# Kernel tuning notes

Measured on AMD Instinct MI355X. Metric: run time of the kernel, lower is better.

## Reference

```python
import jax, jax.numpy as jnp
import numpy as np

N_HEAD = 16
RMS_EPS = 1.1920928955078125e-07  # torch F.rms_norm default eps = finfo(fp32).eps


def _rope_tables(seq_len, head_dim, dtype):
    steps = jnp.arange(seq_len, dtype=jnp.float32)
    rates = 10000.0 ** (-jnp.arange(0, head_dim, 2, dtype=jnp.float32) / head_dim)
    angles = jnp.outer(steps, rates)  # [S, D/2]
    return jnp.cos(angles).astype(dtype)[None, None], jnp.sin(angles).astype(dtype)[None, None]


def _apply_rotary(x, cos, sin):
    # interleaved RoPE: pairs (x[2i], x[2i+1]) rotated
    left = x[..., ::2]
    right = x[..., 1::2]
    lo = left * cos - right * sin
    ro = left * sin + right * cos
    return jnp.stack((lo, ro), axis=-1).reshape(x.shape)


def _rms_norm(x, eps=RMS_EPS):
    ms = jnp.mean(jnp.square(x), axis=-1, keepdims=True)
    return x * jax.lax.rsqrt(ms + eps)


def setup_inputs() -> dict:
    key = jax.random.key(0)
    k1, k2, k3 = jax.random.split(key, 3)
    B, S, E = 2, 2048, 2048
    x = jax.random.normal(k1, (B, S, E), dtype=jnp.float32)
    w_qkv = jax.random.normal(k2, (3 * E, E), dtype=jnp.float32) * (E ** -0.5)
    w_proj = jax.random.normal(k3, (E, E), dtype=jnp.float32) * (E ** -0.5)
    return {"x": x, "w_qkv": w_qkv, "w_proj": w_proj}


def reference(x, w_qkv, w_proj):
    B, S, E = x.shape
    H = N_HEAD
    D = E // H

    qkv = x @ w_qkv.T  # [B, S, 3E]
    q, k, v = jnp.split(qkv, 3, axis=-1)
    # [B, S, E] -> [B, H, S, D]
    q = q.reshape(B, S, H, D).transpose(0, 2, 1, 3)
    k = k.reshape(B, S, H, D).transpose(0, 2, 1, 3)
    v = v.reshape(B, S, H, D).transpose(0, 2, 1, 3)

    cos, sin = _rope_tables(S, D, x.dtype)  # [1,1,S,D/2]
    q = _apply_rotary(q, cos, sin)
    k = _apply_rotary(k, cos, sin)

    q = _rms_norm(q)
    k = _rms_norm(k)

    scale = 1.0 / jnp.sqrt(jnp.asarray(D, dtype=x.dtype))
    scores = jnp.einsum("bhqd,bhkd->bhqk", q, k) * scale  # [B,H,S,S]
    causal = jnp.tril(jnp.ones((S, S), dtype=bool))
    scores = jnp.where(causal[None, None], scores, jnp.asarray(-jnp.inf, dtype=scores.dtype))
    attn = jax.nn.softmax(scores, axis=-1)
    y = jnp.einsum("bhqk,bhkd->bhqd", attn, v)  # [B,H,S,D]
    y = y.transpose(0, 2, 1, 3).reshape(B, S, E)
    return y @ w_proj.T
```

## Files before the change

kernel.cpp:

```cpp
#include <hip/hip_runtime.h>

typedef unsigned short ushort_t;
using bf16x8 = __attribute__((ext_vector_type(8))) short;
using u16x8  = __attribute__((ext_vector_type(8))) unsigned short;
using f32x4  = __attribute__((ext_vector_type(4))) float;

#define DEV static __device__ __forceinline__

DEV unsigned short f2bf(float f) {
  union { float f; unsigned u; } a; a.f = f;
  unsigned r = a.u + 0x7fffu + ((a.u >> 16) & 1u);
  return (unsigned short)(r >> 16);
}
DEV float bf2f(unsigned short u) {
  union { unsigned u; float f; } a; a.u = ((unsigned)u) << 16;
  return a.f;
}
DEV void load_lds16(const void* g, void* l) {
  __builtin_amdgcn_global_load_lds(
      (const __attribute__((address_space(1))) void*)g,
      (__attribute__((address_space(3))) void*)l, 16, 0, 0);
}

__global__ __launch_bounds__(256) void cast_kernel(
    const float* __restrict__ src, ushort_t* __restrict__ dst, int n4) {
  int i = blockIdx.x * 256 + threadIdx.x;
  if (i >= n4) return;
  float4 f = ((const float4*)src)[i];
  ushort4 o;
  o.x = f2bf(f.x); o.y = f2bf(f.y); o.z = f2bf(f.z); o.w = f2bf(f.w);
  ((ushort4*)dst)[i] = o;
}

__global__ __launch_bounds__(256) void rope_tables_kernel(float* __restrict__ tab) {
  int idx = blockIdx.x * 256 + threadIdx.x;
  int s = idx >> 6, i = idx & 63;
  float rate = exp2f(-13.287712379549449f * ((float)(2 * i) * (1.0f / 128.0f)));
  float ang = (float)s * rate;
  tab[idx * 2]     = cosf(ang);
  tab[idx * 2 + 1] = sinf(ang);
}

template<int BN, int OUTF32>
__global__ __launch_bounds__(512) void gemm8p(
    const ushort_t* __restrict__ A, const ushort_t* __restrict__ B,
    void* __restrict__ C, int M, int N, int K) {
  constexpr int NF      = BN / 64;
  constexpr int NSPAN   = BN / 4;
  constexpr int SLOT_A  = 256 * 32;
  constexpr int SLOT_B  = BN * 32;
  constexpr int SLOT    = SLOT_A + SLOT_B;
  constexpr int LOADS_B = BN / 128;
  constexpr int VMC     = (2 + LOADS_B) * 3;
  __shared__ __align__(16) ushort_t lds[4 * SLOT];

  const int nby = M >> 8;
  const int nbx = N / BN;
  const int nwg = nby * nbx;
  const int orig = blockIdx.x;
  const int wgid = (orig & 7) * (nwg >> 3) + (orig >> 3);
  const int by = wgid % nby;
  const int bx = wgid / nby;
  const int bm = by * 256, bn = bx * BN;

  const int tid = threadIdx.x;
  const int wave = tid >> 6, lane = tid & 63;
  const int ql = lane & 15, lk = lane >> 4;
  const int wm = wave >> 2, wn = wave & 3;

  f32x4 acc[8][NF];
#pragma unroll
  for (int m = 0; m < 8; ++m)
#pragma unroll
    for (int n = 0; n < NF; ++n) acc[m][n] = (f32x4){0.f, 0.f, 0.f, 0.f};

  const int srow = tid >> 2;
  const int scol = (tid & 3) * 16;
  const int sswz = scol ^ (((srow >> 1) & 3) << 4);
  const size_t rbA = (size_t)(K * 2);
  const char* aS0 = (const char*)A + (size_t)(bm + srow) * rbA + sswz;
  const char* aS1 = (const char*)A + (size_t)(bm + srow + 128) * rbA + sswz;
  const char* bS0 = (const char*)B + (size_t)(bn + srow) * rbA + sswz;
  const char* bS1 = (const char*)B + (size_t)(bn + srow + 128) * rbA + sswz;
  char* ldsc = (char*)lds;
  const int dA0 = tid * 16;
  const int dA1 = tid * 16 + 8192;
  const int dB0 = SLOT_A * 2 + tid * 16;
  const int dB1 = SLOT_A * 2 + tid * 16 + 8192;

#define ISSUE(KS, SL) do {                                   \
    const size_t ko = (size_t)(KS) * 64;                     \
    char* sb = ldsc + (SL) * (SLOT * 2);                     \
    load_lds16(aS0 + ko, sb + dA0);                          \
    load_lds16(aS1 + ko, sb + dA1);                          \
    load_lds16(bS0 + ko, sb + dB0);                          \
    if (LOADS_B == 2) load_lds16(bS1 + ko, sb + dB1);        \
  } while (0)

  const int qswz = ((ql >> 1) & 3) << 4;
  const int fcol = (lk * 16) ^ qswz;
  const int aOff = (wm * 128 + ql) * 64 + fcol;
  const int bOff = SLOT_A * 2 + (wn * NSPAN + ql) * 64 + fcol;

  const int ns = K >> 5;
  ISSUE(0, 0); ISSUE(1, 1); ISSUE(2, 2);

  for (int s = 0; s < ns; ++s) {
    int kn = s + 3; if (kn >= ns) kn = ns - 1;
    ISSUE(kn, (s + 3) & 3);
    if (VMC == 12) asm volatile("s_waitcnt vmcnt(12)" ::: "memory");
    else           asm volatile("s_waitcnt vmcnt(9)"  ::: "memory");
    asm volatile("s_barrier" ::: "memory");

    const char* sb = ldsc + (s & 3) * (SLOT * 2);
    bf16x8 af[8], bfr[NF];
#pragma unroll
    for (int m = 0; m < 8; ++m) af[m] = *(const bf16x8*)(sb + aOff + m * 1024);
#pragma unroll
    for (int n = 0; n < NF; ++n) bfr[n] = *(const bf16x8*)(sb + bOff + n * 1024);

    __builtin_amdgcn_s_setprio(1);
#pragma unroll
    for (int m = 0; m < 8; ++m)
#pragma unroll
      for (int n = 0; n < NF; ++n)
        acc[m][n] = __builtin_amdgcn_mfma_f32_16x16x32_bf16(af[m], bfr[n], acc[m][n], 0, 0, 0);
    __builtin_amdgcn_s_setprio(0);
    asm volatile("s_barrier" ::: "memory");
  }
  asm volatile("s_waitcnt vmcnt(0)" ::: "memory");
#undef ISSUE

#pragma unroll
  for (int m = 0; m < 8; ++m)
#pragma unroll
    for (int i = 0; i < 4; ++i) {
      const size_t row = (size_t)(bm + wm * 128 + m * 16 + lk * 4 + i);
#pragma unroll
      for (int n = 0; n < NF; ++n) {
        const size_t col = (size_t)(bn + wn * NSPAN + n * 16 + ql);
        float v = acc[m][n][i];
        if (OUTF32) ((float*)C)[row * (size_t)N + col] = v;
        else        ((ushort_t*)C)[row * (size_t)N + col] = f2bf(v);
      }
    }
}

__global__ __launch_bounds__(256) void rope_rms_kernel(
    const ushort_t* __restrict__ qkv, ushort_t* __restrict__ q,
    ushort_t* __restrict__ k, ushort_t* __restrict__ vt,
    const float* __restrict__ tab) {
  const int lane = threadIdx.x & 63;
  const int row  = blockIdx.x * 4 + (threadIdx.x >> 6);
  const int h = row & 15;
  int t = row >> 4;
  const int which = t % 3; t /= 3;
  const int s = t & 2047;
  const int b = t >> 11;
  const size_t src = ((size_t)(b * 2048 + s)) * 6144 + which * 2048 + h * 128 + lane * 2;
  ushort2 xv = *(const ushort2*)&qkv[src];
  if (which == 2) {
    size_t vbase = ((size_t)((b * 16 + h) * 128 + lane * 2)) * 2048 + s;
    vt[vbase]        = xv.x;
    vt[vbase + 2048] = xv.y;
    return;
  }
  float lo = bf2f(xv.x), ro = bf2f(xv.y);
  const float2 cs = *(const float2*)&tab[(s * 64 + lane) * 2];
  float l2 = lo * cs.x - ro * cs.y;
  float r2 = lo * cs.y + ro * cs.x;
  float ss = l2 * l2 + r2 * r2;
#pragma unroll
  for (int off = 1; off < 64; off <<= 1) ss += __shfl_xor(ss, off);
  float inv = rsqrtf(ss * (1.0f / 128.0f) + 1.1920928955078125e-07f);
  if (which == 0) inv *= 0.1275174398f;
  lo = l2 * inv; ro = r2 * inv;
  ushort_t* dst = (which == 0) ? q : k;
  ushort2 o; o.x = f2bf(lo); o.y = f2bf(ro);
  *(ushort2*)&dst[(((size_t)(b * 16 + h)) * 2048 + s) * 128 + lane * 2] = o;
}

__global__ __launch_bounds__(256) void attn_kernel(
    const ushort_t* __restrict__ Q, const ushort_t* __restrict__ K,
    const ushort_t* __restrict__ VT, ushort_t* __restrict__ Y) {
  __shared__ __align__(16) ushort_t sK[64 * 128];
  __shared__ __align__(16) ushort_t sV[128 * 64];
  const int bh = blockIdx.x;
  const int yp = blockIdx.y;
  const int wave = threadIdx.x >> 6, lane = threadIdx.x & 63;
  const int ql = lane & 15, lk = lane >> 4;
  const size_t hq = (size_t)bh * 2048 * 128;
  const int b = bh >> 4, h = bh & 15;

  const char* kB = (const char*)(K + hq);
  const char* vB = (const char*)(VT + hq);
  const char* kSrc[4]; char* kDst[4];
  const char* vSrc[4]; char* vDst[4];
#pragma unroll
  for (int t = 0; t < 4; ++t) {
    int r = wave * 16 + t * 4 + (lane >> 4);
    int kgr = r >> 4, lkr = (r >> 2) & 3, ir = r & 3;
    int rho = (kgr >> 1) * 32 + lkr * 8 + (kgr & 1) * 4 + ir;
    kSrc[t] = kB + rho * 256 + (((lane & 15) * 16) ^ ((r & 7) << 4));
    kDst[t] = (char*)sK + (wave * 256 + t * 64 + lane) * 16;
    int d = wave * 32 + t * 8 + (lane >> 3);
    vSrc[t] = vB + (size_t)d * 4096 + (((lane & 7) * 16) ^ ((d & 7) << 4));
    vDst[t] = (char*)sV + (wave * 256 + t * 64 + lane) * 16;
  }

  for (int pass = 0; pass < 2; ++pass) {
    const int qt = pass ? (31 - yp) : yp;
    const int q = qt * 64 + wave * 16 + ql;

    bf16x8 qf[4];
#pragma unroll
    for (int ks = 0; ks < 4; ++ks)
      qf[ks] = *(const bf16x8*)&Q[hq + (size_t)q * 128 + ks * 32 + lk * 8];

    f32x4 acc[8];
#pragma unroll
    for (int g = 0; g < 8; ++g) acc[g] = (f32x4){0.f, 0.f, 0.f, 0.f};
    float mrow = -3.0e38f, lsum = 0.f;

    for (int kt = 0; kt <= qt; ++kt) {
#pragma unroll
      for (int t = 0; t < 4; ++t) {
        load_lds16(kSrc[t] + (size_t)kt * 16384, kDst[t]);
        load_lds16(vSrc[t] + kt * 128, vDst[t]);
      }
      __syncthreads();

      f32x4 st[4];
#pragma unroll
      for (int kg = 0; kg < 4; ++kg) st[kg] = (f32x4){0.f, 0.f, 0.f, 0.f};
#pragma unroll
      for (int kg = 0; kg < 4; ++kg) {
        const int row = kg * 16 + ql;
        const int rswz = (row & 7) << 4;
#pragma unroll
        for (int ks = 0; ks < 4; ++ks) {
          bf16x8 kf = *(const bf16x8*)((const char*)sK + row * 256 + ((ks * 64 + lk * 16) ^ rswz));
          st[kg] = __builtin_amdgcn_mfma_f32_16x16x32_bf16(kf, qf[ks], st[kg], 0, 0, 0);
        }
      }
      float sv[4][4]; float mp = -3.0e38f;
#pragma unroll
      for (int kg = 0; kg < 4; ++kg) {
        const int kl = ((kg >> 1) << 5) + lk * 8 + ((kg & 1) << 2);
#pragma unroll
        for (int i = 0; i < 4; ++i) {
          const int key = kt * 64 + kl + i;
          float v = (key <= q) ? st[kg][i] : -3.0e38f;
          sv[kg][i] = v;
          mp = fmaxf(mp, v);
        }
      }
      mp = fmaxf(mp, __shfl_xor(mp, 16));
      mp = fmaxf(mp, __shfl_xor(mp, 32));
      const float mn = fmaxf(mrow, mp);
      const float corr = exp2f(mrow - mn);
      mrow = mn;
      float p[4][4]; float rs = 0.f;
#pragma unroll
      for (int kg = 0; kg < 4; ++kg)
#pragma unroll
        for (int i = 0; i < 4; ++i) {
          float e = exp2f(sv[kg][i] - mn);
          p[kg][i] = e; rs += e;
        }
      rs += __shfl_xor(rs, 16);
      rs += __shfl_xor(rs, 32);
      lsum = lsum * corr + rs;
#pragma unroll
      for (int g = 0; g < 8; ++g)
#pragma unroll
        for (int i = 0; i < 4; ++i) acc[g][i] *= corr;
      bf16x8 pb[2];
#pragma unroll
      for (int c = 0; c < 2; ++c) {
        union { bf16x8 v; ushort_t u[8]; } pk;
#pragma unroll
        for (int j = 0; j < 8; ++j) pk.u[j] = f2bf(p[2 * c + (j >> 2)][j & 3]);
        pb[c] = pk.v;
      }
#pragma unroll
      for (int dg = 0; dg < 8; ++dg) {
        const int d = dg * 16 + ql;
        const int dswz = (d & 7) << 4;
#pragma unroll
        for (int c = 0; c < 2; ++c) {
          bf16x8 vf = *(const bf16x8*)((const char*)sV + d * 128 + ((c * 64 + lk * 16) ^ dswz));
          acc[dg] = __builtin_amdgcn_mfma_f32_16x16x32_bf16(vf, pb[c], acc[dg], 0, 0, 0);
        }
      }
      __syncthreads();
    }

    const float inv = 1.0f / lsum;
    const size_t orow = ((size_t)(b * 2048 + q)) * 2048 + h * 128;
#pragma unroll
    for (int dg = 0; dg < 8; ++dg) {
      ushort4 o;
      o.x = f2bf(acc[dg][0] * inv);
      o.y = f2bf(acc[dg][1] * inv);
      o.z = f2bf(acc[dg][2] * inv);
      o.w = f2bf(acc[dg][3] * inv);
      *(ushort4*)&Y[orow + dg * 16 + lk * 4] = o;
    }
  }
}

extern "C" void kernel_launch(void* const* d_in, const int* in_sizes, int n_in,
                              void* d_out, int out_size, void* d_ws, size_t ws_size,
                              hipStream_t stream) {
  const float* x     = (const float*)d_in[0];
  const float* wqkv  = (const float*)d_in[1];
  const float* wproj = (const float*)d_in[2];
  float* out = (float*)d_out;
  char* ws = (char*)d_ws;

  ushort_t* x_bf     = (ushort_t*)(ws);
  ushort_t* wqkv_bf  = (ushort_t*)(ws + 16777216);
  ushort_t* wproj_bf = (ushort_t*)(ws + 41943040);
  ushort_t* qkv_bf   = (ushort_t*)(ws + 50331648);
  ushort_t* q_bf     = (ushort_t*)(ws + 100663296);
  ushort_t* k_bf     = (ushort_t*)(ws + 117440512);
  ushort_t* vt_bf    = (ushort_t*)(ws + 134217728);
  float*    tab      = (float*)(ws + 150994944);
  if (ws_size < 152043520u) return;

  cast_kernel<<<8192, 256, 0, stream>>>(x, x_bf, 2097152);
  cast_kernel<<<12288, 256, 0, stream>>>(wqkv, wqkv_bf, 3145728);
  cast_kernel<<<4096, 256, 0, stream>>>(wproj, wproj_bf, 1048576);
  rope_tables_kernel<<<512, 256, 0, stream>>>(tab);

  gemm8p<256, 0><<<384, 512, 0, stream>>>(x_bf, wqkv_bf, qkv_bf, 4096, 6144, 2048);

  rope_rms_kernel<<<49152, 256, 0, stream>>>(qkv_bf, q_bf, k_bf, vt_bf, tab);

  attn_kernel<<<dim3(32, 16), 256, 0, stream>>>(q_bf, k_bf, vt_bf, qkv_bf );

  gemm8p<128, 1><<<256, 512, 0, stream>>>(qkv_bf, wproj_bf, out, 4096, 2048, 2048);
}
```

Baseline: 317.8 us.

## Double-buffer A fragments in registers and retile GEMM waves

The GEMM main loop now prefetches the next k-step's A fragments from LDS into a second register set while the MFMAs for the current step run, unrolling by two to ping-pong the buffers. The waitcnt is relaxed to allow two outstanding stages. For BN=128 the wave layout changes to 4x2 with 64-row warp tiles, and launch bounds request two blocks per CU. The aim is to hide LDS read latency behind MFMAs, at the cost of more registers, and to better balance the projection GEMM.

```diff
diff --git a/kernel.cpp b/kernel.cpp
--- a/kernel.cpp
+++ b/kernel.cpp
@@ -42,103 +42,119 @@
 }
 
 template<int BN, int OUTF32>
-__global__ __launch_bounds__(512) void gemm8p(
+__global__ __launch_bounds__(512, 2) void gemm_dp(
     const ushort_t* __restrict__ A, const ushort_t* __restrict__ B,
     void* __restrict__ C, int M, int N, int K) {
-  constexpr int NF      = BN / 64;
-  constexpr int NSPAN   = BN / 4;
+  constexpr int WROWS   = (BN == 256) ? 128 : 64;
+  constexpr int MF      = WROWS / 16;
+  constexpr int NF      = 4;
   constexpr int SLOT_A  = 256 * 32;
   constexpr int SLOT_B  = BN * 32;
-  constexpr int SLOT    = SLOT_A + SLOT_B;
+  constexpr int SLOTB   = (SLOT_A + SLOT_B) * 2;
   constexpr int LOADS_B = BN / 128;
-  constexpr int VMC     = (2 + LOADS_B) * 3;
-  __shared__ __align__(16) ushort_t lds[4 * SLOT];
+  __shared__ __align__(16) ushort_t lds[4 * (SLOT_A + SLOT_B)];
 
   const int nby = M >> 8;
-  const int nbx = N / BN;
-  const int nwg = nby * nbx;
+  const int nwg = nby * (N / BN);
   const int orig = blockIdx.x;
   const int wgid = (orig & 7) * (nwg >> 3) + (orig >> 3);
-  const int by = wgid % nby;
-  const int bx = wgid / nby;
-  const int bm = by * 256, bn = bx * BN;
+  const int bm = (wgid % nby) * 256;
+  const int bn = (wgid / nby) * BN;
 
   const int tid = threadIdx.x;
   const int wave = tid >> 6, lane = tid & 63;
   const int ql = lane & 15, lk = lane >> 4;
-  const int wm = wave >> 2, wn = wave & 3;
-
-  f32x4 acc[8][NF];
-#pragma unroll
-  for (int m = 0; m < 8; ++m)
+  const int wm = (BN == 256) ? (wave >> 2) : (wave >> 1);
+  const int wn = (BN == 256) ? (wave & 3) : (wave & 1);
+
+  f32x4 acc[MF][NF];
+#pragma unroll
+  for (int m = 0; m < MF; ++m)
 #pragma unroll
     for (int n = 0; n < NF; ++n) acc[m][n] = (f32x4){0.f, 0.f, 0.f, 0.f};
 
   const int srow = tid >> 2;
-  const int scol = (tid & 3) * 16;
-  const int sswz = scol ^ (((srow >> 1) & 3) << 4);
+  const int sswz = ((tid & 3) * 16) ^ (((srow >> 1) & 3) << 4);
   const size_t rbA = (size_t)(K * 2);
   const char* aS0 = (const char*)A + (size_t)(bm + srow) * rbA + sswz;
   const char* aS1 = (const char*)A + (size_t)(bm + srow + 128) * rbA + sswz;
   const char* bS0 = (const char*)B + (size_t)(bn + srow) * rbA + sswz;
-  const char* bS1 = (const char*)B + (size_t)(bn + srow + 128) * rbA + sswz;
+  const char* bS1 = (LOADS_B == 2)
+      ? (const char*)B + (size_t)(bn + srow + 128) * rbA + sswz : bS0;
   char* ldsc = (char*)lds;
   const int dA0 = tid * 16;
   const int dA1 = tid * 16 + 8192;
   const int dB0 = SLOT_A * 2 + tid * 16;
   const int dB1 = SLOT_A * 2 + tid * 16 + 8192;
 
-#define ISSUE(KS, SL) do {                                   \
-    const size_t ko = (size_t)(KS) * 64;                     \
-    char* sb = ldsc + (SL) * (SLOT * 2);                     \
-    load_lds16(aS0 + ko, sb + dA0);                          \
-    load_lds16(aS1 + ko, sb + dA1);                          \
-    load_lds16(bS0 + ko, sb + dB0);                          \
-    if (LOADS_B == 2) load_lds16(bS1 + ko, sb + dB1);        \
+  const int fcol = (lk * 16) ^ (((ql >> 1) & 3) << 4);
+  const int aOff = (wm * WROWS + ql) * 64 + fcol;
+  const int bOff = SLOT_A * 2 + (wn * 64 + ql) * 64 + fcol;
+
+  const int ns = K >> 5;
+
+#define STEP(S, CUR, NXT) do {                                                  \
+    int kn_ = (S) + 3; if (kn_ > ns - 1) kn_ = ns - 1;                          \
+    const size_t ko_ = (size_t)kn_ * 64;                                        \
+    char* sb_ = ldsc + (((S) + 3) & 3) * SLOTB;                                 \
+    load_lds16(aS0 + ko_, sb_ + dA0);                                           \
+    load_lds16(aS1 + ko_, sb_ + dA1);                                           \
+    load_lds16(bS0 + ko_, sb_ + dB0);                                           \
+    if (LOADS_B == 2) load_lds16(bS1 + ko_, sb_ + dB1);                         \
+    asm volatile("s_waitcnt vmcnt(%0)" :: "n"(2 * (2 + LOADS_B)) : "memory");   \
+    __builtin_amdgcn_s_barrier();                                               \
+    asm volatile("" ::: "memory");                                              \
+    const char* sbc_ = ldsc + ((S) & 3) * SLOTB;                                \
+    const char* sbn_ = ldsc + (((S) + 1) & 3) * SLOTB;                          \
+    bf16x8 bfr_[NF];                                                            \
+    _Pragma("unroll")                                                           \
+    for (int n = 0; n < NF; ++n)                                                \
+      bfr_[n] = *(const bf16x8*)(sbc_ + bOff + n * 1024);                       \
+    _Pragma("unroll")                                                           \
+    for (int m = 0; m < MF; ++m)                                                \
+      NXT[m] = *(const bf16x8*)(sbn_ + aOff + m * 1024);                        \
+    __builtin_amdgcn_s_setprio(1);                                              \
+    _Pragma("unroll")                                                           \
+    for (int n = 0; n < NF; ++n)                                                \
+      _Pragma("unroll")                                                         \
+      for (int m = 0; m < MF; ++m)                                              \
+        acc[m][n] = __builtin_amdgcn_mfma_f32_16x16x32_bf16(CUR[m], bfr_[n],    \
+                                                            acc[m][n], 0, 0, 0);\
+    __builtin_amdgcn_s_setprio(0);                                              \
+    __builtin_amdgcn_s_barrier();                                               \
   } while (0)
 
-  const int qswz = ((ql >> 1) & 3) << 4;
-  const int fcol = (lk * 16) ^ qswz;
-  const int aOff = (wm * 128 + ql) * 64 + fcol;
-  const int bOff = SLOT_A * 2 + (wn * NSPAN + ql) * 64 + fcol;
-
-  const int ns = K >> 5;
-  ISSUE(0, 0); ISSUE(1, 1); ISSUE(2, 2);
-
-  for (int s = 0; s < ns; ++s) {
-    int kn = s + 3; if (kn >= ns) kn = ns - 1;
-    ISSUE(kn, (s + 3) & 3);
-    if (VMC == 12) asm volatile("s_waitcnt vmcnt(12)" ::: "memory");
-    else           asm volatile("s_waitcnt vmcnt(9)"  ::: "memory");
-    asm volatile("s_barrier" ::: "memory");
-
-    const char* sb = ldsc + (s & 3) * (SLOT * 2);
-    bf16x8 af[8], bfr[NF];
-#pragma unroll
-    for (int m = 0; m < 8; ++m) af[m] = *(const bf16x8*)(sb + aOff + m * 1024);
-#pragma unroll
-    for (int n = 0; n < NF; ++n) bfr[n] = *(const bf16x8*)(sb + bOff + n * 1024);
-
-    __builtin_amdgcn_s_setprio(1);
-#pragma unroll
-    for (int m = 0; m < 8; ++m)
-#pragma unroll
-      for (int n = 0; n < NF; ++n)
-        acc[m][n] = __builtin_amdgcn_mfma_f32_16x16x32_bf16(af[m], bfr[n], acc[m][n], 0, 0, 0);
-    __builtin_amdgcn_s_setprio(0);
-    asm volatile("s_barrier" ::: "memory");
+#pragma unroll
+  for (int i = 0; i < 3; ++i) {
+    const size_t ko = (size_t)i * 64;
+    char* sb = ldsc + i * SLOTB;
+    load_lds16(aS0 + ko, sb + dA0);
+    load_lds16(aS1 + ko, sb + dA1);
+    load_lds16(bS0 + ko, sb + dB0);
+    if (LOADS_B == 2) load_lds16(bS1 + ko, sb + dB1);
+  }
+  asm volatile("s_waitcnt vmcnt(%0)" :: "n"(2 * (2 + LOADS_B)) : "memory");
+  __builtin_amdgcn_s_barrier();
+  asm volatile("" ::: "memory");
+  bf16x8 frA[MF], frB[MF];
+#pragma unroll
+  for (int m = 0; m < MF; ++m) frA[m] = *(const bf16x8*)(ldsc + aOff + m * 1024);
+
+  for (int s = 0; s < ns; s += 2) {
+    STEP(s, frA, frB);
+    STEP(s + 1, frB, frA);
   }
   asm volatile("s_waitcnt vmcnt(0)" ::: "memory");
-#undef ISSUE
-
-#pragma unroll
-  for (int m = 0; m < 8; ++m)
+#undef STEP
+
+#pragma unroll
+  for (int m = 0; m < MF; ++m)
 #pragma unroll
     for (int i = 0; i < 4; ++i) {
-      const size_t row = (size_t)(bm + wm * 128 + m * 16 + lk * 4 + i);
+      const size_t row = (size_t)(bm + wm * WROWS + m * 16 + lk * 4 + i);
 #pragma unroll
       for (int n = 0; n < NF; ++n) {
-        const size_t col = (size_t)(bn + wn * NSPAN + n * 16 + ql);
+        const size_t col = (size_t)(bn + wn * 64 + n * 16 + ql);
         float v = acc[m][n][i];
         if (OUTF32) ((float*)C)[row * (size_t)N + col] = v;
         else        ((ushort_t*)C)[row * (size_t)N + col] = f2bf(v);
@@ -334,11 +350,11 @@
   cast_kernel<<<4096, 256, 0, stream>>>(wproj, wproj_bf, 1048576);
   rope_tables_kernel<<<512, 256, 0, stream>>>(tab);
 
-  gemm8p<256, 0><<<384, 512, 0, stream>>>(x_bf, wqkv_bf, qkv_bf, 4096, 6144, 2048);
+  gemm_dp<256, 0><<<384, 512, 0, stream>>>(x_bf, wqkv_bf, qkv_bf, 4096, 6144, 2048);
 
   rope_rms_kernel<<<49152, 256, 0, stream>>>(qkv_bf, q_bf, k_bf, vt_bf, tab);
 
   attn_kernel<<<dim3(32, 16), 256, 0, stream>>>(q_bf, k_bf, vt_bf, qkv_bf );
 
-  gemm8p<128, 1><<<256, 512, 0, stream>>>(qkv_bf, wproj_bf, out, 4096, 2048, 2048);
-}
+  gemm_dp<128, 1><<<256, 512, 0, stream>>>(qkv_bf, wproj_bf, out, 4096, 2048, 2048);
+}
```

Measured after the change: 313.6 us. No clear change (-1.3%).

## Restructure GEMM into double-buffered 64-wide K tiles with interleaved load/MFMA phases

Applied to the files above, without the earlier changes.

Replaces the 4-stage ring buffer of 32-wide K slices with a 2-buffer pipeline over 64-wide K tiles. Each tile is split into four MFMA phases, with LDS fragment reads and the next tile's global-to-LDS loads interleaved between barriers. The LDS swizzle changes to an 8-way XOR over 128-byte rows, and launch bounds request 2 workgroups per CU. This aims to hide load latency and raise MFMA utilisation. In exchange it adds many more barriers, and occupancy 2 may be limited by LDS size and register count. An unused mfma16 prototype is declared but never defined.

```diff
diff --git a/kernel.cpp b/kernel.cpp
--- a/kernel.cpp
+++ b/kernel.cpp
@@ -21,6 +21,7 @@
       (const __attribute__((address_space(1))) void*)g,
       (__attribute__((address_space(3))) void*)l, 16, 0, 0);
 }
+DEV bf16x8 mfma16(bf16x8 a, bf16x8 b);
 
 __global__ __launch_bounds__(256) void cast_kernel(
     const float* __restrict__ src, ushort_t* __restrict__ dst, int n4) {
@@ -42,29 +43,25 @@
 }
 
 template<int BN, int OUTF32>
-__global__ __launch_bounds__(512) void gemm8p(
-    const ushort_t* __restrict__ A, const ushort_t* __restrict__ B,
+__global__ __launch_bounds__(512, 2) void gemm8(
+    const ushort_t* __restrict__ A, const ushort_t* __restrict__ Bm,
     void* __restrict__ C, int M, int N, int K) {
-  constexpr int NF      = BN / 64;
-  constexpr int NSPAN   = BN / 4;
-  constexpr int SLOT_A  = 256 * 32;
-  constexpr int SLOT_B  = BN * 32;
-  constexpr int SLOT    = SLOT_A + SLOT_B;
-  constexpr int LOADS_B = BN / 128;
-  constexpr int VMC     = (2 + LOADS_B) * 3;
-  __shared__ __align__(16) ushort_t lds[4 * SLOT];
+  constexpr int NF   = BN / 64;
+  constexpr int ABY  = 256 * 64 * 2;
+  constexpr int BBY  = BN * 64 * 2;
+  constexpr int BUFB = ABY + BBY;
+  __shared__ __align__(16) char lds[2 * BUFB];
 
   const int nby = M >> 8;
-  const int nbx = N / BN;
-  const int nwg = nby * nbx;
+  const int nwg = nby * (N / BN);
   const int orig = blockIdx.x;
   const int wgid = (orig & 7) * (nwg >> 3) + (orig >> 3);
-  const int by = wgid % nby;
-  const int bx = wgid / nby;
-  const int bm = by * 256, bn = bx * BN;
+  const int bm = (wgid % nby) * 256;
+  const int bn = (wgid / nby) * BN;
 
   const int tid = threadIdx.x;
-  const int wave = tid >> 6, lane = tid & 63;
+  const int lane = tid & 63;
+  const int wave = tid >> 6;
   const int ql = lane & 15, lk = lane >> 4;
   const int wm = wave >> 2, wn = wave & 3;
 
@@ -74,62 +71,172 @@
 #pragma unroll
     for (int n = 0; n < NF; ++n) acc[m][n] = (f32x4){0.f, 0.f, 0.f, 0.f};
 
-  const int srow = tid >> 2;
-  const int scol = (tid & 3) * 16;
-  const int sswz = scol ^ (((srow >> 1) & 3) << 4);
-  const size_t rbA = (size_t)(K * 2);
-  const char* aS0 = (const char*)A + (size_t)(bm + srow) * rbA + sswz;
-  const char* aS1 = (const char*)A + (size_t)(bm + srow + 128) * rbA + sswz;
-  const char* bS0 = (const char*)B + (size_t)(bn + srow) * rbA + sswz;
-  const char* bS1 = (const char*)B + (size_t)(bn + srow + 128) * rbA + sswz;
-  char* ldsc = (char*)lds;
-  const int dA0 = tid * 16;
-  const int dA1 = tid * 16 + 8192;
-  const int dB0 = SLOT_A * 2 + tid * 16;
-  const int dB1 = SLOT_A * 2 + tid * 16 + 8192;
-
-#define ISSUE(KS, SL) do {                                   \
-    const size_t ko = (size_t)(KS) * 64;                     \
-    char* sb = ldsc + (SL) * (SLOT * 2);                     \
-    load_lds16(aS0 + ko, sb + dA0);                          \
-    load_lds16(aS1 + ko, sb + dA1);                          \
-    load_lds16(bS0 + ko, sb + dB0);                          \
-    if (LOADS_B == 2) load_lds16(bS1 + ko, sb + dB1);        \
-  } while (0)
-
-  const int qswz = ((ql >> 1) & 3) << 4;
-  const int fcol = (lk * 16) ^ qswz;
-  const int aOff = (wm * 128 + ql) * 64 + fcol;
-  const int bOff = SLOT_A * 2 + (wn * NSPAN + ql) * 64 + fcol;
-
-  const int ns = K >> 5;
-  ISSUE(0, 0); ISSUE(1, 1); ISSUE(2, 2);
-
-  for (int s = 0; s < ns; ++s) {
-    int kn = s + 3; if (kn >= ns) kn = ns - 1;
-    ISSUE(kn, (s + 3) & 3);
-    if (VMC == 12) asm volatile("s_waitcnt vmcnt(12)" ::: "memory");
-    else           asm volatile("s_waitcnt vmcnt(9)"  ::: "memory");
-    asm volatile("s_barrier" ::: "memory");
-
-    const char* sb = ldsc + (s & 3) * (SLOT * 2);
-    bf16x8 af[8], bfr[NF];
-#pragma unroll
-    for (int m = 0; m < 8; ++m) af[m] = *(const bf16x8*)(sb + aOff + m * 1024);
-#pragma unroll
-    for (int n = 0; n < NF; ++n) bfr[n] = *(const bf16x8*)(sb + bOff + n * 1024);
-
-    __builtin_amdgcn_s_setprio(1);
-#pragma unroll
-    for (int m = 0; m < 8; ++m)
-#pragma unroll
-      for (int n = 0; n < NF; ++n)
-        acc[m][n] = __builtin_amdgcn_mfma_f32_16x16x32_bf16(af[m], bfr[n], acc[m][n], 0, 0, 0);
-    __builtin_amdgcn_s_setprio(0);
-    asm volatile("s_barrier" ::: "memory");
+  const int srow = tid >> 3;
+  const int scol = ((tid & 7) ^ (srow & 7)) * 16;
+  const size_t rb = (size_t)K * 2;
+  const char* aS[4];
+#pragma unroll
+  for (int c = 0; c < 4; ++c)
+    aS[c] = (const char*)A + (size_t)(bm + c * 64 + srow) * rb + scol;
+  const char* bS[NF];
+#pragma unroll
+  for (int c = 0; c < NF; ++c)
+    bS[c] = (const char*)Bm + (size_t)(bn + c * 64 + srow) * rb + scol;
+  char* const ldsc = (char*)lds;
+  const int dT = tid * 16;
+
+  const int aRow = wm * 128 + ql;
+  const int bRow = wn * (BN / 4) + ql;
+  const int qx = ql & 7;
+
+#define RDA(BUF, m, kh) \
+  (*(const bf16x8*)((BUF) + (aRow + (m) * 16) * 128 + ((((kh) << 2) | lk) ^ qx) * 16))
+#define RDB(BUF, n, kh) \
+  (*(const bf16x8*)((BUF) + ABY + (bRow + (n) * 16) * 128 + ((((kh) << 2) | lk) ^ qx) * 16))
+#define STGA(BUF, KT, c) load_lds16(aS[c] + (size_t)(KT) * 128, (BUF) + (c) * 8192 + dT)
+#define STGB(BUF, KT, c) load_lds16(bS[c] + (size_t)(KT) * 128, (BUF) + ABY + (c) * 8192 + dT)
+#define MFMA(a, b, c) __builtin_amdgcn_mfma_f32_16x16x32_bf16(a, b, c, 0, 0, 0)
+
+  const int ns = K >> 6;
+
+  STGA(ldsc, 0, 0); STGA(ldsc, 0, 2);
+  STGB(ldsc, 0, 0); STGB(ldsc, 0, 1);
+  if constexpr (NF == 4) { STGB(ldsc, 0, 2); STGB(ldsc, 0, 3); }
+  STGA(ldsc, 0, 1); STGA(ldsc, 0, 3);
+  asm volatile("s_waitcnt vmcnt(2)" ::: "memory");
+  __builtin_amdgcn_s_barrier();
+
+  for (int t = 0; t < ns; ++t) {
+    char* bufR = ldsc + (t & 1) * BUFB;
+    char* bufW = ldsc + ((t + 1) & 1) * BUFB;
+    const int kn = (t + 1 < ns) ? t + 1 : ns - 1;
+
+    if constexpr (NF == 4) {
+      bf16x8 aF[4][2], bF[4][2];
+#pragma unroll
+      for (int mi = 0; mi < 4; ++mi) {
+        aF[mi][0] = RDA(bufR, mi, 0); aF[mi][1] = RDA(bufR, mi, 1);
+      }
+#pragma unroll
+      for (int n = 0; n < 2; ++n) {
+        bF[n][0] = RDB(bufR, n, 0); bF[n][1] = RDB(bufR, n, 1);
+      }
+      STGA(bufW, kn, 0); STGA(bufW, kn, 2);
+      STGB(bufW, kn, 0); STGB(bufW, kn, 1); STGB(bufW, kn, 2); STGB(bufW, kn, 3);
+      __builtin_amdgcn_s_barrier();
+      __builtin_amdgcn_s_setprio(1);
+#pragma unroll
+      for (int n = 0; n < 2; ++n)
+#pragma unroll
+        for (int kh = 0; kh < 2; ++kh)
+#pragma unroll
+          for (int mi = 0; mi < 4; ++mi)
+            acc[mi][n] = MFMA(aF[mi][kh], bF[n][kh], acc[mi][n]);
+      __builtin_amdgcn_s_setprio(0);
+      __builtin_amdgcn_s_barrier();
+#pragma unroll
+      for (int n = 2; n < 4; ++n) {
+        bF[n][0] = RDB(bufR, n, 0); bF[n][1] = RDB(bufR, n, 1);
+      }
+      asm volatile("s_waitcnt vmcnt(6)" ::: "memory");
+      __builtin_amdgcn_s_barrier();
+      __builtin_amdgcn_s_setprio(1);
+#pragma unroll
+      for (int n = 2; n < 4; ++n)
+#pragma unroll
+        for (int kh = 0; kh < 2; ++kh)
+#pragma unroll
+          for (int mi = 0; mi < 4; ++mi)
+            acc[mi][n] = MFMA(aF[mi][kh], bF[n][kh], acc[mi][n]);
+      __builtin_amdgcn_s_setprio(0);
+      __builtin_amdgcn_s_barrier();
+#pragma unroll
+      for (int mi = 0; mi < 4; ++mi) {
+        aF[mi][0] = RDA(bufR, 4 + mi, 0); aF[mi][1] = RDA(bufR, 4 + mi, 1);
+      }
+      STGA(bufW, kn, 1); STGA(bufW, kn, 3);
+      __builtin_amdgcn_s_barrier();
+      __builtin_amdgcn_s_setprio(1);
+#pragma unroll
+      for (int n = 0; n < 2; ++n)
+#pragma unroll
+        for (int kh = 0; kh < 2; ++kh)
+#pragma unroll
+          for (int mi = 0; mi < 4; ++mi)
+            acc[4 + mi][n] = MFMA(aF[mi][kh], bF[n][kh], acc[4 + mi][n]);
+      __builtin_amdgcn_s_setprio(0);
+      __builtin_amdgcn_s_barrier();
+      __builtin_amdgcn_s_setprio(1);
+#pragma unroll
+      for (int n = 2; n < 4; ++n)
+#pragma unroll
+        for (int kh = 0; kh < 2; ++kh)
+#pragma unroll
+          for (int mi = 0; mi < 4; ++mi)
+            acc[4 + mi][n] = MFMA(aF[mi][kh], bF[n][kh], acc[4 + mi][n]);
+      __builtin_amdgcn_s_setprio(0);
+      asm volatile("s_waitcnt vmcnt(2)" ::: "memory");
+      __builtin_amdgcn_s_barrier();
+    } else {
+      bf16x8 aF0[4], aF1[4], bF[2][2];
+#pragma unroll
+      for (int mi = 0; mi < 4; ++mi) aF0[mi] = RDA(bufR, mi, 0);
+      bF[0][0] = RDB(bufR, 0, 0); bF[1][0] = RDB(bufR, 1, 0);
+      STGA(bufW, kn, 0); STGA(bufW, kn, 2);
+      STGB(bufW, kn, 0); STGB(bufW, kn, 1);
+      __builtin_amdgcn_s_barrier();
+      __builtin_amdgcn_s_setprio(1);
+#pragma unroll
+      for (int n = 0; n < 2; ++n)
+#pragma unroll
+        for (int mi = 0; mi < 4; ++mi)
+          acc[mi][n] = MFMA(aF0[mi], bF[n][0], acc[mi][n]);
+      __builtin_amdgcn_s_setprio(0);
+      __builtin_amdgcn_s_barrier();
+#pragma unroll
+      for (int mi = 0; mi < 4; ++mi) aF1[mi] = RDA(bufR, mi, 1);
+      bF[0][1] = RDB(bufR, 0, 1); bF[1][1] = RDB(bufR, 1, 1);
+      asm volatile("s_waitcnt vmcnt(4)" ::: "memory");
+      __builtin_amdgcn_s_barrier();
+      __builtin_amdgcn_s_setprio(1);
+#pragma unroll
+      for (int n = 0; n < 2; ++n)
+#pragma unroll
+        for (int mi = 0; mi < 4; ++mi)
+          acc[mi][n] = MFMA(aF1[mi], bF[n][1], acc[mi][n]);
+      __builtin_amdgcn_s_setprio(0);
+      __builtin_amdgcn_s_barrier();
+#pragma unroll
+      for (int mi = 0; mi < 4; ++mi) aF0[mi] = RDA(bufR, 4 + mi, 0);
+      STGA(bufW, kn, 1); STGA(bufW, kn, 3);
+      __builtin_amdgcn_s_barrier();
+      __builtin_amdgcn_s_setprio(1);
+#pragma unroll
+      for (int n = 0; n < 2; ++n)
+#pragma unroll
+        for (int mi = 0; mi < 4; ++mi)
+          acc[4 + mi][n] = MFMA(aF0[mi], bF[n][0], acc[4 + mi][n]);
+      __builtin_amdgcn_s_setprio(0);
+      __builtin_amdgcn_s_barrier();
+#pragma unroll
+      for (int mi = 0; mi < 4; ++mi) aF1[mi] = RDA(bufR, 4 + mi, 1);
+      __builtin_amdgcn_s_barrier();
+      __builtin_amdgcn_s_setprio(1);
+#pragma unroll
+      for (int n = 0; n < 2; ++n)
+#pragma unroll
+        for (int mi = 0; mi < 4; ++mi)
+          acc[4 + mi][n] = MFMA(aF1[mi], bF[n][1], acc[4 + mi][n]);
+      __builtin_amdgcn_s_setprio(0);
+      asm volatile("s_waitcnt vmcnt(2)" ::: "memory");
+      __builtin_amdgcn_s_barrier();
+    }
   }
-  asm volatile("s_waitcnt vmcnt(0)" ::: "memory");
-#undef ISSUE
+#undef RDA
+#undef RDB
+#undef STGA
+#undef STGB
+#undef MFMA
 
 #pragma unroll
   for (int m = 0; m < 8; ++m)
@@ -138,7 +245,7 @@
       const size_t row = (size_t)(bm + wm * 128 + m * 16 + lk * 4 + i);
 #pragma unroll
       for (int n = 0; n < NF; ++n) {
-        const size_t col = (size_t)(bn + wn * NSPAN + n * 16 + ql);
+        const size_t col = (size_t)(bn + wn * (BN / 4) + n * 16 + ql);
         float v = acc[m][n][i];
         if (OUTF32) ((float*)C)[row * (size_t)N + col] = v;
         else        ((ushort_t*)C)[row * (size_t)N + col] = f2bf(v);
@@ -334,11 +441,11 @@
   cast_kernel<<<4096, 256, 0, stream>>>(wproj, wproj_bf, 1048576);
   rope_tables_kernel<<<512, 256, 0, stream>>>(tab);
 
-  gemm8p<256, 0><<<384, 512, 0, stream>>>(x_bf, wqkv_bf, qkv_bf, 4096, 6144, 2048);
+  gemm8<256, 0><<<384, 512, 0, stream>>>(x_bf, wqkv_bf, qkv_bf, 4096, 6144, 2048);
 
   rope_rms_kernel<<<49152, 256, 0, stream>>>(qkv_bf, q_bf, k_bf, vt_bf, tab);
 
   attn_kernel<<<dim3(32, 16), 256, 0, stream>>>(q_bf, k_bf, vt_bf, qkv_bf );
 
-  gemm8p<128, 1><<<256, 512, 0, stream>>>(qkv_bf, wproj_bf, out, 4096, 2048, 2048);
-}
+  gemm8<128, 1><<<256, 512, 0, stream>>>(qkv_bf, wproj_bf, out, 4096, 2048, 2048);
+}
```

Result: faster. 307.8 us (-3.2%).
